# Optimization experiments

Measured on AMD Instinct MI355X. Metric: run time of the kernel, lower is better.

## Reference

```python
import jax, jax.numpy as jnp
import numpy as np

N_NODES = 100000
N_EDGES = 1600000
N_GRAPHS = 64
D_IN = 3
HIDDEN = 256
N_CLASSES = 10
NEG_SLOPE = 0.01  # torch F.leaky_relu default


def gcn_conv(x, W, b, src, dst, n_nodes):
    """GCNConv: D^{-1/2}(A+I)D^{-1/2} X W + b with self-loops."""
    h = x @ W  # [N, H]
    ones = jnp.ones(src.shape[0], h.dtype)
    deg = jax.ops.segment_sum(ones, dst, num_segments=n_nodes) + 1.0  # +1 self-loop
    dinv = jax.lax.rsqrt(deg)
    coef = dinv[src] * dinv[dst]  # [E]
    agg = jax.ops.segment_sum(h[src] * coef[:, None], dst, num_segments=n_nodes)
    agg = agg + h * (1.0 / deg)[:, None]  # self-loop contribution (norm = 1/deg)
    return agg + b


def leaky_relu(v):
    return jnp.where(v >= 0, v, NEG_SLOPE * v)


def setup_inputs() -> dict:
    key = jax.random.key(0)
    ks = jax.random.split(key, 12)
    x = jax.random.normal(ks[0], (N_NODES, D_IN), dtype=jnp.float32)
    edge_index = jax.random.randint(ks[1], (2, N_EDGES), 0, N_NODES, dtype=jnp.int32)
    batch = jnp.sort(jax.random.randint(ks[2], (N_NODES,), 0, N_GRAPHS, dtype=jnp.int32))
    s1 = 1.0 / np.sqrt(D_IN)
    s2 = 1.0 / np.sqrt(HIDDEN)
    W1 = jax.random.uniform(ks[3], (D_IN, HIDDEN), jnp.float32, -s1, s1)
    b1 = jnp.zeros((HIDDEN,), jnp.float32)
    W2 = jax.random.uniform(ks[4], (HIDDEN, HIDDEN), jnp.float32, -s2, s2)
    b2 = jnp.zeros((HIDDEN,), jnp.float32)
    W3 = jax.random.uniform(ks[5], (HIDDEN, HIDDEN), jnp.float32, -s2, s2)
    b3 = jnp.zeros((HIDDEN,), jnp.float32)
    Wc = jax.random.uniform(ks[6], (HIDDEN, N_CLASSES), jnp.float32, -s2, s2)
    bc = jax.random.uniform(ks[7], (N_CLASSES,), jnp.float32, -s2, s2)
    return {"x": x, "edge_index": edge_index, "batch": batch,
            "W1": W1, "b1": b1, "W2": W2, "b2": b2, "W3": W3, "b3": b3,
            "Wc": Wc, "bc": bc}


def reference(x, edge_index, batch, W1, b1, W2, b2, W3, b3, Wc, bc):
    src, dst = edge_index[0], edge_index[1]
    h = leaky_relu(gcn_conv(x, W1, b1, src, dst, N_NODES))
    h = leaky_relu(gcn_conv(h, W2, b2, src, dst, N_NODES))
    h = leaky_relu(gcn_conv(h, W3, b3, src, dst, N_NODES))
    # global mean pool over graphs
    sums = jax.ops.segment_sum(h, batch, num_segments=N_GRAPHS)
    cnt = jax.ops.segment_sum(jnp.ones((N_NODES,), h.dtype), batch, num_segments=N_GRAPHS)
    pooled = sums / jnp.maximum(cnt, 1.0)[:, None]  # [G, H]
    logits = pooled @ Wc + bc
    return jax.nn.softmax(logits, axis=1)
```

## Files before the change

kernel.cpp:

```cpp
#include <hip/hip_runtime.h>
#include <hip/hip_bf16.h>
#include <hip/hip_fp16.h>
#include <cstdint>
#include <cstddef>

#define N_NODES   100000
#define N_EDGES   1600000
#define N_GRAPHS  64
#define HIDDEN    256
#define N_CLASSES 10
#define NEG_SLOPE 0.01f

#define E_PAD    (N_EDGES + 8 * N_NODES)
#define N_RANGES 8
#define R_SIZE   ((N_NODES + N_RANGES - 1) / N_RANGES)
#define GEMM_BLOCKS 391

#define PART_EDGES  8192
#define PART_BLOCKS ((N_EDGES + PART_EDGES - 1) / PART_EDGES)
#define RB_CHUNKS   108
#define CAP_R       (RB_CHUNKS * 2048)

typedef __attribute__((ext_vector_type(4))) float f32x4;
typedef __attribute__((ext_vector_type(2))) float f32x2;

__device__ __forceinline__ float bf2f(unsigned short u) {
    return __uint_as_float(((unsigned int)u) << 16);
}

__device__ __forceinline__ unsigned char f2fp8(float v) {
    return (unsigned char)(__builtin_amdgcn_cvt_pk_fp8_f32(v, v, 0, false) & 0xff);
}

__device__ __forceinline__ unsigned int rec_pack(int s, float c) {
    __half h = __float2half(c);
    unsigned short hb = reinterpret_cast<const __half_raw*>(&h)->x;
    return ((unsigned int)hb << 17) | (unsigned int)s;
}
__device__ __forceinline__ float rec_coef(unsigned int u) {
    __half_raw hr; hr.x = (unsigned short)(u >> 17);
    return __half2float(*reinterpret_cast<const __half*>(&hr));
}

__global__ __launch_bounds__(256) void k_partition(const int* __restrict__ src, const int* __restrict__ dst,
                                                   int* __restrict__ gcur, unsigned int* __restrict__ bucket) {
    __shared__ int lcnt[8];
    __shared__ int lbase[8];
    __shared__ int gbase[8];
    __shared__ unsigned int stage[PART_EDGES];
    int tid = threadIdx.x;
    if (tid < 8) lcnt[tid] = 0;
    __syncthreads();
    int e0 = blockIdx.x * PART_EDGES + tid * 8;
    for (int g = 0; g < 4; ++g) {
        int e = e0 + g * 2048;
        if (e < N_EDGES) {
            int4 da = *(const int4*)(dst + e);
            int4 db = *(const int4*)(dst + e + 4);
            int d[8] = {da.x, da.y, da.z, da.w, db.x, db.y, db.z, db.w};
#pragma unroll
            for (int j = 0; j < 8; ++j) atomicAdd(&lcnt[d[j] / R_SIZE], 1);
        }
    }
    __syncthreads();
    if (tid == 0) {
        int s = 0;
        for (int r = 0; r < 8; ++r) { lbase[r] = s; s += lcnt[r]; }
    }
    __syncthreads();
    if (tid < 8) {
        gbase[tid] = atomicAdd(&gcur[tid * 16], lcnt[tid]);
        lcnt[tid] = lbase[tid];
    }
    __syncthreads();
    for (int g = 0; g < 4; ++g) {
        int e = e0 + g * 2048;
        if (e < N_EDGES) {
            int4 da = *(const int4*)(dst + e);
            int4 db = *(const int4*)(dst + e + 4);
            int4 sa = *(const int4*)(src + e);
            int4 sb = *(const int4*)(src + e + 4);
            int d[8] = {da.x, da.y, da.z, da.w, db.x, db.y, db.z, db.w};
            int s[8] = {sa.x, sa.y, sa.z, sa.w, sb.x, sb.y, sb.z, sb.w};
#pragma unroll
            for (int j = 0; j < 8; ++j) {
                int r = d[j] / R_SIZE;
                int p = atomicAdd(&lcnt[r], 1);
                stage[p] = ((unsigned int)(d[j] - r * R_SIZE) << 17) | (unsigned int)s[j];
            }
        }
    }
    __syncthreads();
    for (int r = 0; r < 8; ++r) {
        int base = lbase[r], n = lcnt[r] - base, gb = gbase[r];
        unsigned int* dp = bucket + (size_t)r * CAP_R + gb;
        for (int k = tid; k < n; k += 256) dp[k] = stage[base + k];
    }
}

__global__ __launch_bounds__(256) void k_hist2(const unsigned int* __restrict__ bucket,
                                               const int* __restrict__ gcur,
                                               int* __restrict__ cnt, unsigned char* __restrict__ rankb) {
    int b = blockIdx.x;
    int r = b & 7, chunk = b >> 3;
    int n = gcur[r * 16];
    int i0 = chunk * 2048 + threadIdx.x * 8;
    if (i0 >= n) return;
    const unsigned int* bp = bucket + (size_t)r * CAP_R;
    uint4 ua = *(const uint4*)(bp + i0);
    uint4 ub = *(const uint4*)(bp + i0 + 4);
    unsigned int u[8] = {ua.x, ua.y, ua.z, ua.w, ub.x, ub.y, ub.z, ub.w};
    int lo = r * R_SIZE;
    int m = n - i0; if (m > 8) m = 8;
    unsigned long long pk = 0;
#pragma unroll
    for (int j = 0; j < 8; ++j) {
        if (j < m) {
            int d = lo + (int)(u[j] >> 17);
            unsigned int rk = (unsigned int)atomicAdd(&cnt[d], 1);
            pk |= (unsigned long long)(rk & 0xff) << (8 * j);
        }
    }
    *(unsigned long long*)(rankb + (size_t)r * CAP_R + i0) = pk;
}

__global__ __launch_bounds__(256) void k_fill2(const unsigned int* __restrict__ bucket,
                                               const unsigned char* __restrict__ rankb,
                                               const int* __restrict__ gcur,
                                               const float* __restrict__ dinv,
                                               const int* __restrict__ off,
                                               unsigned int* __restrict__ rec) {
    int b = blockIdx.x;
    int r = b & 7, chunk = b >> 3;
    int n = gcur[r * 16];
    int i0 = chunk * 2048 + threadIdx.x * 8;
    if (i0 >= n) return;
    const unsigned int* bp = bucket + (size_t)r * CAP_R;
    uint4 ua = *(const uint4*)(bp + i0);
    uint4 ub = *(const uint4*)(bp + i0 + 4);
    unsigned long long rk8 = *(const unsigned long long*)(rankb + (size_t)r * CAP_R + i0);
    unsigned int u[8] = {ua.x, ua.y, ua.z, ua.w, ub.x, ub.y, ub.z, ub.w};
    int lo = r * R_SIZE;
    int m = n - i0; if (m > 8) m = 8;
#pragma unroll
    for (int j = 0; j < 8; ++j) {
        if (j < m) {
            int s = (int)(u[j] & 0x1ffff);
            int d = lo + (int)(u[j] >> 17);
            float c = dinv[s] * dinv[d];
            int p = off[d] + (int)((rk8 >> (8 * j)) & 0xff);
            rec[p] = rec_pack(s, c);
        }
    }
}

__global__ void k_graph_bounds(const int* __restrict__ batch,
                               int* __restrict__ gstart, int* __restrict__ gcnt) {
    int g = threadIdx.x;
    int lo = 0, hi = N_NODES;
    while (lo < hi) { int mid = (lo + hi) >> 1; if (batch[mid] < g) lo = mid + 1; else hi = mid; }
    __shared__ int sh[N_GRAPHS + 1];
    sh[g] = lo;
    if (g == 0) sh[N_GRAPHS] = N_NODES;
    __syncthreads();
    gstart[g] = sh[g];
    gcnt[g]   = sh[g + 1] - sh[g];
}

__global__ void k_dinv_xpad(const int* __restrict__ cnt, const float* __restrict__ x,
                            float* __restrict__ dinv, float4* __restrict__ xp) {
    int i = blockIdx.x * 256 + threadIdx.x;
    if (i < N_NODES) {
        dinv[i] = rsqrtf((float)cnt[i] + 1.0f);
        xp[i] = make_float4(x[i * 3 + 0], x[i * 3 + 1], x[i * 3 + 2], 0.f);
    }
}

__global__ void k_scanA(const int* __restrict__ cnt, int* __restrict__ out, int* __restrict__ bsum) {
    __shared__ int sh[256];
    int tid = threadIdx.x;
    int base = blockIdx.x * 1024 + tid * 4;
    int v[4]; int s = 0;
#pragma unroll
    for (int i = 0; i < 4; i++) {
        int idx = base + i;
        v[i] = (idx < N_NODES) ? ((cnt[idx] + 7) & ~7) : 0;
        s += v[i];
    }
    sh[tid] = s; __syncthreads();
    for (int off = 1; off < 256; off <<= 1) {
        int t = (tid >= off) ? sh[tid - off] : 0;
        __syncthreads();
        sh[tid] += t;
        __syncthreads();
    }
    int excl = sh[tid] - s;
    if (tid == 255) bsum[blockIdx.x] = sh[255];
#pragma unroll
    for (int i = 0; i < 4; i++) { int idx = base + i; if (idx < N_NODES) out[idx] = excl; excl += v[i]; }
}

__global__ void k_scanB(int* __restrict__ bsum, int nb) {
    __shared__ int sh[128];
    int tid = threadIdx.x;
    int v = (tid < nb) ? bsum[tid] : 0;
    sh[tid] = v; __syncthreads();
    for (int off = 1; off < 128; off <<= 1) {
        int t = (tid >= off) ? sh[tid - off] : 0;
        __syncthreads();
        sh[tid] += t;
        __syncthreads();
    }
    if (tid < nb) bsum[tid] = sh[tid] - v;
}

__global__ void k_scanC(int* __restrict__ off_arr, const int* __restrict__ bsum,
                        const int* __restrict__ cnt, unsigned int* __restrict__ rec) {
    int i = blockIdx.x * 256 + threadIdx.x;
    if (i < N_NODES) {
        int v = off_arr[i] + bsum[i >> 10];
        off_arr[i] = v;
        int c  = cnt[i];
        int cp = (c + 7) & ~7;
        for (int p = v + c; p < v + cp; ++p) rec[p] = 0u;
        if (i == N_NODES - 1) off_arr[N_NODES] = v + cp;
    }
}

__global__ void k_wprep(const float* __restrict__ W, unsigned char* __restrict__ Wswz) {
    int n = blockIdx.x; int k = threadIdx.x;
    unsigned char v = f2fp8(W[k * HIDDEN + n]);
    int k0 = k >> 5, nt = n >> 4;
    int lane = (((k >> 3) & 3) << 4) | (n & 15);
    int j = k & 7;
    Wswz[(size_t)(((k0 * 16) + nt) * 64 + lane) * 8 + j] = v;
}

__global__ void k_agg3(const float4* __restrict__ xp, const int* __restrict__ off,
                       const unsigned int* __restrict__ rec, const float* __restrict__ dinv,
                       float4* __restrict__ ax) {
    int i = blockIdx.x * 256 + threadIdx.x;
    if (i >= N_NODES) return;
    float di = dinv[i];
    float selfc = di * di;
    float4 xi = xp[i];
    float a0 = xi.x * selfc, a1 = xi.y * selfc, a2 = xi.z * selfc;
    int e = off[i], e1 = off[i + 1];
    for (; e < e1; e += 4) {
        uint4 rr = *(const uint4*)(rec + e);
        int s0 = rr.x & 0x1ffff, s1 = rr.y & 0x1ffff, s2 = rr.z & 0x1ffff, s3 = rr.w & 0x1ffff;
        float c0 = rec_coef(rr.x), c1 = rec_coef(rr.y), c2 = rec_coef(rr.z), c3 = rec_coef(rr.w);
        float4 x0 = xp[s0], x1 = xp[s1], x2 = xp[s2], x3 = xp[s3];
        a0 += c0 * x0.x + c1 * x1.x + c2 * x2.x + c3 * x3.x;
        a1 += c0 * x0.y + c1 * x1.y + c2 * x2.y + c3 * x3.y;
        a2 += c0 * x0.z + c1 * x1.z + c2 * x2.z + c3 * x3.z;
    }
    ax[i] = make_float4(a0, a1, a2, 0.f);
}

__global__ void k_l1(const float4* __restrict__ ax, const float* __restrict__ W1,
                     const float* __restrict__ b1, unsigned char* __restrict__ out) {
    int node = blockIdx.x; int c = threadIdx.x;
    float4 a = ax[node];
    float v = a.x * W1[c] + a.y * W1[HIDDEN + c] + a.z * W1[2 * HIDDEN + c] + b1[c];
    v = v >= 0.f ? v : NEG_SLOPE * v;
    out[(size_t)node * HIDDEN + c] = f2fp8(v);
}

__global__ __launch_bounds__(512, 2) void k_gemm_mfma(const unsigned char* __restrict__ A,
                                                      const unsigned char* __restrict__ Wswz,
                                                      unsigned char* __restrict__ C, int M) {
    __shared__ long Bs[8192];
    int tid = threadIdx.x;
    {
        const float4* gsrc = (const float4*)Wswz;
        float4* ldst = (float4*)Bs;
#pragma unroll
        for (int i = 0; i < 8; ++i) ldst[tid + 512 * i] = gsrc[tid + 512 * i];
    }
    __syncthreads();
    int lane = tid & 63, wv = tid >> 6;
    int quad = lane >> 4, r = lane & 15;
    int nstrips = M >> 4;
    for (int s = blockIdx.x * 8 + wv; s < nstrips; s += gridDim.x * 8) {
        int m0 = s * 16;
        const long* Ab = (const long*)(A + (size_t)(m0 + r) * HIDDEN) + quad;
        long af[8];
#pragma unroll
        for (int k0 = 0; k0 < 8; ++k0) af[k0] = Ab[k0 * 4];
#pragma unroll
        for (int half = 0; half < 2; ++half) {
            f32x4 acc[8];
#pragma unroll
            for (int i = 0; i < 8; i++) acc[i] = (f32x4){0.f, 0.f, 0.f, 0.f};
#pragma unroll
            for (int k0 = 0; k0 < 8; ++k0) {
#pragma unroll
                for (int nt = 0; nt < 8; ++nt) {
                    long b = Bs[(k0 * 16 + half * 8 + nt) * 64 + lane];
                    acc[nt] = __builtin_amdgcn_mfma_f32_16x16x32_fp8_fp8(af[k0], b, acc[nt], 0, 0, 0);
                }
            }
#pragma unroll
            for (int nt = 0; nt < 8; ++nt) {
#pragma unroll
                for (int i = 0; i < 4; ++i) {
                    int row = m0 + quad * 4 + i;
                    C[(size_t)row * HIDDEN + (half * 8 + nt) * 16 + r] = f2fp8(acc[nt][i]);
                }
            }
        }
    }
}

__global__ __launch_bounds__(256) void k_agg(const unsigned char* __restrict__ h,
                                             const float* __restrict__ bias,
                                             const int* __restrict__ off, const unsigned int* __restrict__ rec,
                                             const float* __restrict__ dinv,
                                             unsigned char* __restrict__ out) {
    int node = (blockIdx.x * 256 + threadIdx.x) >> 6;
    int lane = threadIdx.x & 63;
    if (node >= N_NODES) return;
    float di = dinv[node];
    float selfc = di * di;
    unsigned int hv = *(const unsigned int*)(h + (size_t)node * HIDDEN + lane * 4);
    f32x2 hlo = __builtin_amdgcn_cvt_pk_f32_fp8(hv, false);
    f32x2 hhi = __builtin_amdgcn_cvt_pk_f32_fp8(hv, true);
    float4 bv = ((const float4*)bias)[lane];
    float4 acc = make_float4(bv.x + hlo.x * selfc, bv.y + hlo.y * selfc,
                             bv.z + hhi.x * selfc, bv.w + hhi.y * selfc);
    int e = off[node], e1 = off[node + 1];
    for (; e < e1; e += 8) {
        uint4 ra = *(const uint4*)(rec + e);
        uint4 rb = *(const uint4*)(rec + e + 4);
        unsigned int w0 = *(const unsigned int*)(h + (size_t)(ra.x & 0x1ffff) * HIDDEN + lane * 4);
        unsigned int w1 = *(const unsigned int*)(h + (size_t)(ra.y & 0x1ffff) * HIDDEN + lane * 4);
        unsigned int w2 = *(const unsigned int*)(h + (size_t)(ra.z & 0x1ffff) * HIDDEN + lane * 4);
        unsigned int w3 = *(const unsigned int*)(h + (size_t)(ra.w & 0x1ffff) * HIDDEN + lane * 4);
        unsigned int w4 = *(const unsigned int*)(h + (size_t)(rb.x & 0x1ffff) * HIDDEN + lane * 4);
        unsigned int w5 = *(const unsigned int*)(h + (size_t)(rb.y & 0x1ffff) * HIDDEN + lane * 4);
        unsigned int w6 = *(const unsigned int*)(h + (size_t)(rb.z & 0x1ffff) * HIDDEN + lane * 4);
        unsigned int w7 = *(const unsigned int*)(h + (size_t)(rb.w & 0x1ffff) * HIDDEN + lane * 4);
        float c0 = rec_coef(ra.x), c1 = rec_coef(ra.y), c2 = rec_coef(ra.z), c3 = rec_coef(ra.w);
        float c4 = rec_coef(rb.x), c5 = rec_coef(rb.y), c6 = rec_coef(rb.z), c7 = rec_coef(rb.w);
        f32x2 l0 = __builtin_amdgcn_cvt_pk_f32_fp8(w0, false), g0 = __builtin_amdgcn_cvt_pk_f32_fp8(w0, true);
        f32x2 l1 = __builtin_amdgcn_cvt_pk_f32_fp8(w1, false), g1 = __builtin_amdgcn_cvt_pk_f32_fp8(w1, true);
        f32x2 l2 = __builtin_amdgcn_cvt_pk_f32_fp8(w2, false), g2 = __builtin_amdgcn_cvt_pk_f32_fp8(w2, true);
        f32x2 l3 = __builtin_amdgcn_cvt_pk_f32_fp8(w3, false), g3 = __builtin_amdgcn_cvt_pk_f32_fp8(w3, true);
        f32x2 l4 = __builtin_amdgcn_cvt_pk_f32_fp8(w4, false), g4 = __builtin_amdgcn_cvt_pk_f32_fp8(w4, true);
        f32x2 l5 = __builtin_amdgcn_cvt_pk_f32_fp8(w5, false), g5 = __builtin_amdgcn_cvt_pk_f32_fp8(w5, true);
        f32x2 l6 = __builtin_amdgcn_cvt_pk_f32_fp8(w6, false), g6 = __builtin_amdgcn_cvt_pk_f32_fp8(w6, true);
        f32x2 l7 = __builtin_amdgcn_cvt_pk_f32_fp8(w7, false), g7 = __builtin_amdgcn_cvt_pk_f32_fp8(w7, true);
        acc.x += c0 * l0.x + c1 * l1.x + c2 * l2.x + c3 * l3.x
               + c4 * l4.x + c5 * l5.x + c6 * l6.x + c7 * l7.x;
        acc.y += c0 * l0.y + c1 * l1.y + c2 * l2.y + c3 * l3.y
               + c4 * l4.y + c5 * l5.y + c6 * l6.y + c7 * l7.y;
        acc.z += c0 * g0.x + c1 * g1.x + c2 * g2.x + c3 * g3.x
               + c4 * g4.x + c5 * g5.x + c6 * g6.x + c7 * g7.x;
        acc.w += c0 * g0.y + c1 * g1.y + c2 * g2.y + c3 * g3.y
               + c4 * g4.y + c5 * g5.y + c6 * g6.y + c7 * g7.y;
    }
    acc.x = acc.x >= 0.f ? acc.x : NEG_SLOPE * acc.x;
    acc.y = acc.y >= 0.f ? acc.y : NEG_SLOPE * acc.y;
    acc.z = acc.z >= 0.f ? acc.z : NEG_SLOPE * acc.z;
    acc.w = acc.w >= 0.f ? acc.w : NEG_SLOPE * acc.w;
    unsigned int pk = __builtin_amdgcn_cvt_pk_fp8_f32(acc.x, acc.y, 0, false);
    pk = __builtin_amdgcn_cvt_pk_fp8_f32(acc.z, acc.w, pk, true);
    *(unsigned int*)(out + (size_t)node * HIDDEN + lane * 4) = pk;
}

__global__ void k_pool(const unsigned char* __restrict__ h, const int* __restrict__ gstart,
                       const int* __restrict__ gcnt, float* __restrict__ pooled) {
    int g = blockIdx.x, chunk = blockIdx.y, t = threadIdx.x;
    int s = gstart[g], c = gcnt[g];
    int i0 = s + (int)(((long long)c * chunk) / 16);
    int i1 = s + (int)(((long long)c * (chunk + 1)) / 16);
    float acc = 0.f;
    for (int i = i0; i < i1; ++i) {
        f32x2 v = __builtin_amdgcn_cvt_pk_f32_fp8((unsigned int)h[(size_t)i * HIDDEN + t], false);
        acc += v.x;
    }
    atomicAdd(&pooled[g * HIDDEN + t], acc);
}

__global__ void k_head(const float* __restrict__ pooled, const int* __restrict__ gcnt,
                       const float* __restrict__ Wc, const float* __restrict__ bc,
                       float* __restrict__ out) {
    int g = blockIdx.x; int l = threadIdx.x;
    float inv = 1.0f / fmaxf((float)gcnt[g], 1.0f);
    float p[4];
#pragma unroll
    for (int i = 0; i < 4; i++) p[i] = pooled[g * HIDDEN + l + i * 64] * inv;
    __shared__ float logits[N_CLASSES];
#pragma unroll
    for (int j = 0; j < N_CLASSES; j++) {
        float s = 0.f;
#pragma unroll
        for (int i = 0; i < 4; i++) s += p[i] * Wc[(l + i * 64) * N_CLASSES + j];
        for (int o = 32; o > 0; o >>= 1) s += __shfl_down(s, o, 64);
        if (l == 0) logits[j] = s + bc[j];
    }
    __syncthreads();
    if (l == 0) {
        float m = logits[0];
        for (int j = 1; j < N_CLASSES; j++) m = fmaxf(m, logits[j]);
        float e[N_CLASSES]; float sum = 0.f;
        for (int j = 0; j < N_CLASSES; j++) { e[j] = expf(logits[j] - m); sum += e[j]; }
        for (int j = 0; j < N_CLASSES; j++) out[g * N_CLASSES + j] = e[j] / sum;
    }
}

extern "C" void kernel_launch(void* const* d_in, const int* in_sizes, int n_in,
                              void* d_out, int out_size, void* d_ws, size_t ws_size,
                              hipStream_t stream) {
    const float* x     = (const float*)d_in[0];
    const int*   edge  = (const int*)d_in[1];
    const int*   batch = (const int*)d_in[2];
    const float* W1 = (const float*)d_in[3];
    const float* b1 = (const float*)d_in[4];
    const float* W2 = (const float*)d_in[5];
    const float* b2 = (const float*)d_in[6];
    const float* W3 = (const float*)d_in[7];
    const float* b3 = (const float*)d_in[8];
    const float* Wc = (const float*)d_in[9];
    const float* bc = (const float*)d_in[10];
    float* out = (float*)d_out;
    const int* srcp = edge;
    const int* dstp = edge + N_EDGES;

    char* ws = (char*)d_ws;
    size_t off = 0;
    auto alloc = [&](size_t bytes) -> char* {
        char* p = ws + off;
        off += (bytes + 255) & ~(size_t)255;
        return p;
    };
    unsigned char* hA   = (unsigned char*)alloc((size_t)N_NODES * HIDDEN);
    unsigned char* hB   = (unsigned char*)alloc((size_t)N_NODES * HIDDEN);
    unsigned char* Wz2  = (unsigned char*)alloc((size_t)HIDDEN * HIDDEN);
    unsigned char* Wz3  = (unsigned char*)alloc((size_t)HIDDEN * HIDDEN);
    int*   deg_cnt  = (int*)alloc((size_t)N_NODES * 4);
    float* dinv     = (float*)alloc((size_t)N_NODES * 4);
    int*   csr_off  = (int*)alloc((size_t)(N_NODES + 1) * 4);
    unsigned int* csr_rec = (unsigned int*)alloc((size_t)E_PAD * 4);
    float4* ax      = (float4*)alloc((size_t)N_NODES * 16);
    float4* xp      = (float4*)alloc((size_t)N_NODES * 16);
    int*   gcnt     = (int*)alloc((size_t)N_GRAPHS * 4);
    int*   gstart   = (int*)alloc((size_t)N_GRAPHS * 4);
    float* pooled   = (float*)alloc((size_t)N_GRAPHS * HIDDEN * 4);
    int*   bsum     = (int*)alloc(128 * 4);
    int*   gcur     = (int*)alloc(128 * 4);

    unsigned int*  bucket = (unsigned int*)hB;
    unsigned char* rankb  = (unsigned char*)(hB + (size_t)8 * CAP_R * 4);

    hipMemsetAsync(deg_cnt, 0, (size_t)N_NODES * 4, stream);
    hipMemsetAsync(gcur, 0, 128 * 4, stream);
    hipMemsetAsync(pooled, 0, (size_t)N_GRAPHS * HIDDEN * 4, stream);

    int nb  = (N_NODES + 255) / 256;
    int sblocks = (N_NODES + 1023) / 1024;
    int rbgrid = RB_CHUNKS * N_RANGES;

    k_partition<<<PART_BLOCKS, 256, 0, stream>>>(srcp, dstp, gcur, bucket);
    k_graph_bounds<<<1, 64, 0, stream>>>(batch, gstart, gcnt);
    k_hist2<<<rbgrid, 256, 0, stream>>>(bucket, gcur, deg_cnt, rankb);
    k_dinv_xpad<<<nb, 256, 0, stream>>>(deg_cnt, x, dinv, xp);
    k_scanA<<<sblocks, 256, 0, stream>>>(deg_cnt, csr_off, bsum);
    k_scanB<<<1, 128, 0, stream>>>(bsum, sblocks);
    k_scanC<<<nb, 256, 0, stream>>>(csr_off, bsum, deg_cnt, csr_rec);
    k_fill2<<<rbgrid, 256, 0, stream>>>(bucket, rankb, gcur, dinv, csr_off, csr_rec);
    k_wprep<<<HIDDEN, HIDDEN, 0, stream>>>(W2, Wz2);
    k_wprep<<<HIDDEN, HIDDEN, 0, stream>>>(W3, Wz3);

    k_agg3<<<nb, 256, 0, stream>>>(xp, csr_off, csr_rec, dinv, ax);
    k_l1<<<N_NODES, 256, 0, stream>>>(ax, W1, b1, hA);

    int aggb = (N_NODES + 3) / 4;
    k_gemm_mfma<<<GEMM_BLOCKS, 512, 0, stream>>>(hA, Wz2, hB, N_NODES);
    k_agg<<<aggb, 256, 0, stream>>>(hB, b2, csr_off, csr_rec, dinv, hA);
    k_gemm_mfma<<<GEMM_BLOCKS, 512, 0, stream>>>(hA, Wz3, hB, N_NODES);
    k_agg<<<aggb, 256, 0, stream>>>(hB, b3, csr_off, csr_rec, dinv, hA);
    dim3 pg(N_GRAPHS, 16);
    k_pool<<<pg, 256, 0, stream>>>(hA, gstart, gcnt, pooled);
    k_head<<<N_GRAPHS, 64, 0, stream>>>(pooled, gcnt, Wc, bc, out);
}
```

Before: 509.3 us.

## Partition edges into 1024-node sub-buckets; LDS histogram and fill; packed fp8 GEMM stores

Edge partitioning now uses 98 sub-ranges of 1024 destination nodes instead of 8 ranges. This lets the degree histogram and CSR fill run per sub-range with LDS atomics and cached offsets and dinv, replacing global atomics and the separate rank buffer. The deg_cnt memset is dropped because the histogram writes counts directly. The MFMA GEMM swaps operands so each lane holds four consecutive output columns, and writes packed 4-byte fp8 stores instead of byte scatters. Risks include bucket overflow if a sub-range exceeds CAP_SUB, and a non-deterministic edge order within rows.

Measured after the change: 478.5 us. 1.06x faster.

```diff
diff --git a/kernel.cpp b/kernel.cpp
--- a/kernel.cpp
+++ b/kernel.cpp
@@ -12,14 +12,14 @@
 #define NEG_SLOPE 0.01f
 
 #define E_PAD    (N_EDGES + 8 * N_NODES)
-#define N_RANGES 8
-#define R_SIZE   ((N_NODES + N_RANGES - 1) / N_RANGES)
 #define GEMM_BLOCKS 391
 
 #define PART_EDGES  8192
 #define PART_BLOCKS ((N_EDGES + PART_EDGES - 1) / PART_EDGES)
-#define RB_CHUNKS   108
-#define CAP_R       (RB_CHUNKS * 2048)
+#define SUB_BITS 10
+#define SUB_SIZE 1024
+#define N_SUB    ((N_NODES + SUB_SIZE - 1) / SUB_SIZE)
+#define CAP_SUB  17408
 
 typedef __attribute__((ext_vector_type(4))) float f32x4;
 typedef __attribute__((ext_vector_type(2))) float f32x2;
@@ -44,12 +44,12 @@
 
 __global__ __launch_bounds__(256) void k_partition(const int* __restrict__ src, const int* __restrict__ dst,
                                                    int* __restrict__ gcur, unsigned int* __restrict__ bucket) {
-    __shared__ int lcnt[8];
-    __shared__ int lbase[8];
-    __shared__ int gbase[8];
+    __shared__ int lcnt[N_SUB];
+    __shared__ int lbase[N_SUB];
+    __shared__ int gbase[N_SUB];
     __shared__ unsigned int stage[PART_EDGES];
     int tid = threadIdx.x;
-    if (tid < 8) lcnt[tid] = 0;
+    for (int i = tid; i < N_SUB; i += 256) lcnt[i] = 0;
     __syncthreads();
     int e0 = blockIdx.x * PART_EDGES + tid * 8;
     for (int g = 0; g < 4; ++g) {
@@ -59,18 +59,18 @@
             int4 db = *(const int4*)(dst + e + 4);
             int d[8] = {da.x, da.y, da.z, da.w, db.x, db.y, db.z, db.w};
 #pragma unroll
-            for (int j = 0; j < 8; ++j) atomicAdd(&lcnt[d[j] / R_SIZE], 1);
+            for (int j = 0; j < 8; ++j) atomicAdd(&lcnt[d[j] >> SUB_BITS], 1);
         }
     }
     __syncthreads();
     if (tid == 0) {
         int s = 0;
-        for (int r = 0; r < 8; ++r) { lbase[r] = s; s += lcnt[r]; }
-    }
-    __syncthreads();
-    if (tid < 8) {
-        gbase[tid] = atomicAdd(&gcur[tid * 16], lcnt[tid]);
-        lcnt[tid] = lbase[tid];
+        for (int r = 0; r < N_SUB; ++r) { lbase[r] = s; s += lcnt[r]; }
+    }
+    __syncthreads();
+    for (int i = tid; i < N_SUB; i += 256) {
+        gbase[i] = atomicAdd(&gcur[i * 16], lcnt[i]);
+        lcnt[i] = lbase[i];
     }
     __syncthreads();
     for (int g = 0; g < 4; ++g) {
@@ -84,72 +84,79 @@
             int s[8] = {sa.x, sa.y, sa.z, sa.w, sb.x, sb.y, sb.z, sb.w};
 #pragma unroll
             for (int j = 0; j < 8; ++j) {
-                int r = d[j] / R_SIZE;
+                int r = d[j] >> SUB_BITS;
                 int p = atomicAdd(&lcnt[r], 1);
-                stage[p] = ((unsigned int)(d[j] - r * R_SIZE) << 17) | (unsigned int)s[j];
+                stage[p] = ((unsigned int)(d[j] & (SUB_SIZE - 1)) << 17) | (unsigned int)s[j];
             }
         }
     }
     __syncthreads();
-    for (int r = 0; r < 8; ++r) {
+    int wv = tid >> 6, ln = tid & 63;
+    for (int r = wv; r < N_SUB; r += 4) {
         int base = lbase[r], n = lcnt[r] - base, gb = gbase[r];
-        unsigned int* dp = bucket + (size_t)r * CAP_R + gb;
-        for (int k = tid; k < n; k += 256) dp[k] = stage[base + k];
-    }
-}
-
-__global__ __launch_bounds__(256) void k_hist2(const unsigned int* __restrict__ bucket,
-                                               const int* __restrict__ gcur,
-                                               int* __restrict__ cnt, unsigned char* __restrict__ rankb) {
-    int b = blockIdx.x;
-    int r = b & 7, chunk = b >> 3;
-    int n = gcur[r * 16];
-    int i0 = chunk * 2048 + threadIdx.x * 8;
-    if (i0 >= n) return;
-    const unsigned int* bp = bucket + (size_t)r * CAP_R;
-    uint4 ua = *(const uint4*)(bp + i0);
-    uint4 ub = *(const uint4*)(bp + i0 + 4);
-    unsigned int u[8] = {ua.x, ua.y, ua.z, ua.w, ub.x, ub.y, ub.z, ub.w};
-    int lo = r * R_SIZE;
-    int m = n - i0; if (m > 8) m = 8;
-    unsigned long long pk = 0;
-#pragma unroll
-    for (int j = 0; j < 8; ++j) {
-        if (j < m) {
-            int d = lo + (int)(u[j] >> 17);
-            unsigned int rk = (unsigned int)atomicAdd(&cnt[d], 1);
-            pk |= (unsigned long long)(rk & 0xff) << (8 * j);
-        }
-    }
-    *(unsigned long long*)(rankb + (size_t)r * CAP_R + i0) = pk;
-}
-
-__global__ __launch_bounds__(256) void k_fill2(const unsigned int* __restrict__ bucket,
-                                               const unsigned char* __restrict__ rankb,
+        unsigned int* dp = bucket + (size_t)r * CAP_SUB + gb;
+        for (int k = ln; k < n; k += 64) dp[k] = stage[base + k];
+    }
+}
+
+__global__ __launch_bounds__(512) void k_hist3(const unsigned int* __restrict__ bucket,
+                                               const int* __restrict__ gcur, int* __restrict__ cnt) {
+    int sub = blockIdx.x;
+    __shared__ int hist[SUB_SIZE];
+    for (int i = threadIdx.x; i < SUB_SIZE; i += 512) hist[i] = 0;
+    __syncthreads();
+    int n = gcur[sub * 16];
+    const unsigned int* bp = bucket + (size_t)sub * CAP_SUB;
+    for (int i0 = threadIdx.x * 8; i0 < n; i0 += 512 * 8) {
+        uint4 ua = *(const uint4*)(bp + i0);
+        uint4 ub = *(const uint4*)(bp + i0 + 4);
+        unsigned int u[8] = {ua.x, ua.y, ua.z, ua.w, ub.x, ub.y, ub.z, ub.w};
+        int m = n - i0; if (m > 8) m = 8;
+#pragma unroll
+        for (int j = 0; j < 8; ++j) if (j < m) atomicAdd(&hist[u[j] >> 17], 1);
+    }
+    __syncthreads();
+    int base = sub * SUB_SIZE;
+    for (int i = threadIdx.x; i < SUB_SIZE; i += 512)
+        if (base + i < N_NODES) cnt[base + i] = hist[i];
+}
+
+__global__ __launch_bounds__(512) void k_fill3(const unsigned int* __restrict__ bucket,
                                                const int* __restrict__ gcur,
                                                const float* __restrict__ dinv,
                                                const int* __restrict__ off,
                                                unsigned int* __restrict__ rec) {
-    int b = blockIdx.x;
-    int r = b & 7, chunk = b >> 3;
-    int n = gcur[r * 16];
-    int i0 = chunk * 2048 + threadIdx.x * 8;
-    if (i0 >= n) return;
-    const unsigned int* bp = bucket + (size_t)r * CAP_R;
-    uint4 ua = *(const uint4*)(bp + i0);
-    uint4 ub = *(const uint4*)(bp + i0 + 4);
-    unsigned long long rk8 = *(const unsigned long long*)(rankb + (size_t)r * CAP_R + i0);
-    unsigned int u[8] = {ua.x, ua.y, ua.z, ua.w, ub.x, ub.y, ub.z, ub.w};
-    int lo = r * R_SIZE;
-    int m = n - i0; if (m > 8) m = 8;
-#pragma unroll
-    for (int j = 0; j < 8; ++j) {
-        if (j < m) {
-            int s = (int)(u[j] & 0x1ffff);
-            int d = lo + (int)(u[j] >> 17);
-            float c = dinv[s] * dinv[d];
-            int p = off[d] + (int)((rk8 >> (8 * j)) & 0xff);
-            rec[p] = rec_pack(s, c);
+    int sub = blockIdx.x;
+    __shared__ int lcur[SUB_SIZE];
+    __shared__ float ldv[SUB_SIZE];
+    int nb0 = sub * SUB_SIZE;
+    for (int i = threadIdx.x; i < SUB_SIZE; i += 512) {
+        int node = nb0 + i;
+        lcur[i] = (node < N_NODES) ? off[node] : 0;
+        ldv[i]  = (node < N_NODES) ? dinv[node] : 0.f;
+    }
+    __syncthreads();
+    int n = gcur[sub * 16];
+    const unsigned int* bp = bucket + (size_t)sub * CAP_SUB;
+    for (int i0 = threadIdx.x * 8; i0 < n; i0 += 512 * 8) {
+        uint4 ua = *(const uint4*)(bp + i0);
+        uint4 ub = *(const uint4*)(bp + i0 + 4);
+        unsigned int u[8] = {ua.x, ua.y, ua.z, ua.w, ub.x, ub.y, ub.z, ub.w};
+        int m = n - i0; if (m > 8) m = 8;
+        float ds[8];
+#pragma unroll
+        for (int j = 0; j < 8; ++j) {
+            int s = (j < m) ? (int)(u[j] & 0x1ffff) : 0;
+            ds[j] = dinv[s];
+        }
+#pragma unroll
+        for (int j = 0; j < 8; ++j) {
+            if (j < m) {
+                int dr = (int)(u[j] >> 17);
+                float c = ds[j] * ldv[dr];
+                int p = atomicAdd(&lcur[dr], 1);
+                rec[p] = rec_pack((int)(u[j] & 0x1ffff), c);
+            }
         }
     }
 }
@@ -288,27 +295,23 @@
         long af[8];
 #pragma unroll
         for (int k0 = 0; k0 < 8; ++k0) af[k0] = Ab[k0 * 4];
-#pragma unroll
-        for (int half = 0; half < 2; ++half) {
-            f32x4 acc[8];
-#pragma unroll
-            for (int i = 0; i < 8; i++) acc[i] = (f32x4){0.f, 0.f, 0.f, 0.f};
-#pragma unroll
-            for (int k0 = 0; k0 < 8; ++k0) {
-#pragma unroll
-                for (int nt = 0; nt < 8; ++nt) {
-                    long b = Bs[(k0 * 16 + half * 8 + nt) * 64 + lane];
-                    acc[nt] = __builtin_amdgcn_mfma_f32_16x16x32_fp8_fp8(af[k0], b, acc[nt], 0, 0, 0);
-                }
+        f32x4 acc[16];
+#pragma unroll
+        for (int i = 0; i < 16; i++) acc[i] = (f32x4){0.f, 0.f, 0.f, 0.f};
+#pragma unroll
+        for (int k0 = 0; k0 < 8; ++k0) {
+#pragma unroll
+            for (int nt = 0; nt < 16; ++nt) {
+                long w = Bs[(k0 * 16 + nt) * 64 + lane];
+                acc[nt] = __builtin_amdgcn_mfma_f32_16x16x32_fp8_fp8(w, af[k0], acc[nt], 0, 0, 0);
             }
-#pragma unroll
-            for (int nt = 0; nt < 8; ++nt) {
-#pragma unroll
-                for (int i = 0; i < 4; ++i) {
-                    int row = m0 + quad * 4 + i;
-                    C[(size_t)row * HIDDEN + (half * 8 + nt) * 16 + r] = f2fp8(acc[nt][i]);
-                }
-            }
+        }
+        unsigned int* crow = (unsigned int*)(C + (size_t)(m0 + r) * HIDDEN + quad * 4);
+#pragma unroll
+        for (int nt = 0; nt < 16; ++nt) {
+            unsigned int pk = __builtin_amdgcn_cvt_pk_fp8_f32(acc[nt][0], acc[nt][1], 0, false);
+            pk = __builtin_amdgcn_cvt_pk_fp8_f32(acc[nt][2], acc[nt][3], pk, true);
+            crow[nt * 4] = pk;
         }
     }
 }
@@ -449,27 +452,24 @@
     int*   gstart   = (int*)alloc((size_t)N_GRAPHS * 4);
     float* pooled   = (float*)alloc((size_t)N_GRAPHS * HIDDEN * 4);
     int*   bsum     = (int*)alloc(128 * 4);
-    int*   gcur     = (int*)alloc(128 * 4);
-
-    unsigned int*  bucket = (unsigned int*)hB;
-    unsigned char* rankb  = (unsigned char*)(hB + (size_t)8 * CAP_R * 4);
-
-    hipMemsetAsync(deg_cnt, 0, (size_t)N_NODES * 4, stream);
-    hipMemsetAsync(gcur, 0, 128 * 4, stream);
+    int*   gcur     = (int*)alloc((size_t)N_SUB * 16 * 4);
+
+    unsigned int* bucket = (unsigned int*)hB;
+
+    hipMemsetAsync(gcur, 0, (size_t)N_SUB * 16 * 4, stream);
     hipMemsetAsync(pooled, 0, (size_t)N_GRAPHS * HIDDEN * 4, stream);
 
     int nb  = (N_NODES + 255) / 256;
     int sblocks = (N_NODES + 1023) / 1024;
-    int rbgrid = RB_CHUNKS * N_RANGES;
 
     k_partition<<<PART_BLOCKS, 256, 0, stream>>>(srcp, dstp, gcur, bucket);
     k_graph_bounds<<<1, 64, 0, stream>>>(batch, gstart, gcnt);
-    k_hist2<<<rbgrid, 256, 0, stream>>>(bucket, gcur, deg_cnt, rankb);
+    k_hist3<<<N_SUB, 512, 0, stream>>>(bucket, gcur, deg_cnt);
     k_dinv_xpad<<<nb, 256, 0, stream>>>(deg_cnt, x, dinv, xp);
     k_scanA<<<sblocks, 256, 0, stream>>>(deg_cnt, csr_off, bsum);
     k_scanB<<<1, 128, 0, stream>>>(bsum, sblocks);
     k_scanC<<<nb, 256, 0, stream>>>(csr_off, bsum, deg_cnt, csr_rec);
-    k_fill2<<<rbgrid, 256, 0, stream>>>(bucket, rankb, gcur, dinv, csr_off, csr_rec);
+    k_fill3<<<N_SUB, 512, 0, stream>>>(bucket, gcur, dinv, csr_off, csr_rec);
     k_wprep<<<HIDDEN, HIDDEN, 0, stream>>>(W2, Wz2);
     k_wprep<<<HIDDEN, HIDDEN, 0, stream>>>(W3, Wz3);
 
```
